# Kernel optimization log

Measured on AMD Instinct MI355X. Metric: run time of the kernel, lower is better.

## Reference

```python
import jax, jax.numpy as jnp
import numpy as np
import math

DIM = 1024
HEADS = 16
WINDOW = 256  # window_size; also used as block size (band covers 3 blocks)


def _rope(x):
    # canonical half-split RoPE over the FULL feature dim (as the module applies
    # it before the head split), base 10000
    b, s, d = x.shape
    half = d // 2
    inv_freq = 1.0 / (10000.0 ** (jnp.arange(half, dtype=jnp.float32) / half))
    ang = jnp.arange(s, dtype=jnp.float32)[:, None] * inv_freq[None, :]  # [s, half]
    cos, sin = jnp.cos(ang), jnp.sin(ang)
    x1, x2 = x[..., :half], x[..., half:]
    return jnp.concatenate([x1 * cos - x2 * sin, x1 * sin + x2 * cos], axis=-1)


def setup_inputs() -> dict:
    key = jax.random.key(0)
    ks = jax.random.split(key, 8)
    d = DIM
    q = jax.random.normal(ks[0], (2, 4096, d), dtype=jnp.float32)
    k = jax.random.normal(ks[1], (2, 4096, d), dtype=jnp.float32)
    v = jax.random.normal(ks[2], (2, 4096, d), dtype=jnp.float32)
    wq = jax.random.normal(ks[3], (d, d), dtype=jnp.float32) * 0.02
    wk = jax.random.normal(ks[4], (d, d), dtype=jnp.float32) * 0.02
    wv = jax.random.normal(ks[5], (d, d), dtype=jnp.float32) * 0.02
    wo_w = jax.random.normal(ks[6], (d, d), dtype=jnp.float32) * 0.02
    wo_b = jnp.zeros((d,), dtype=jnp.float32)
    return {"q": q, "k": k, "v": v, "wq": wq, "wk": wk, "wv": wv,
            "wo_w": wo_w, "wo_b": wo_b}


def reference(q, k, v, wq, wk, wv, wo_w, wo_b):
    b, s, d = q.shape
    h, W = HEADS, WINDOW
    dk = d // h
    B = W                      # block size == window -> band of 3 blocks
    nb = s // B

    # projections (torch Linear: x @ W^T), then RoPE over the full dim
    qp = _rope(jnp.einsum('bsd,ed->bse', q, wq))
    kp = _rope(jnp.einsum('bsd,ed->bse', k, wk))
    vp = jnp.einsum('bsd,ed->bse', v, wv)

    # split heads -> [b, h, s, dk]
    qh = qp.reshape(b, s, h, dk).transpose(0, 2, 1, 3)
    kh = kp.reshape(b, s, h, dk).transpose(0, 2, 1, 3)
    vh = vp.reshape(b, s, h, dk).transpose(0, 2, 1, 3)

    # pad keys/values by one block on each side, gather 3-block bands
    kpad = jnp.pad(kh, ((0, 0), (0, 0), (B, B), (0, 0)))
    vpad = jnp.pad(vh, ((0, 0), (0, 0), (B, B), (0, 0)))
    kblk = kpad.reshape(b, h, nb + 2, B, dk)
    vblk = vpad.reshape(b, h, nb + 2, B, dk)
    kband = jnp.concatenate([kblk[:, :, i:i + nb] for i in range(3)], axis=3)  # [b,h,nb,3B,dk]
    vband = jnp.concatenate([vblk[:, :, i:i + nb] for i in range(3)], axis=3)

    qb = qh.reshape(b, h, nb, B, dk)
    # NOTE: original multiplies by sqrt(dim_k) (not divides) -- kept faithfully
    scores = jnp.einsum('bhnqd,bhnkd->bhnqk', qb, kband) * math.sqrt(dk)

    # band mask: key global pos = (n-1)*B + ki, query global pos = n*B + qi
    n_idx = jnp.arange(nb)[:, None, None]
    qi = jnp.arange(B)[None, :, None]
    ki = jnp.arange(3 * B)[None, None, :]
    kpos = (n_idx - 1) * B + ki
    rel = ki - B - qi  # key_pos - query_pos
    valid = (rel >= -W) & (rel <= W) & (kpos >= 0) & (kpos < s)  # [nb,B,3B]

    neg = jnp.asarray(jnp.finfo(scores.dtype).min, scores.dtype)
    scores = jnp.where(valid[None, None], scores, neg)
    attn = jax.nn.softmax(scores, axis=-1)

    out = jnp.einsum('bhnqk,bhnkd->bhnqd', attn, vband)
    out = out.reshape(b, h, s, dk).transpose(0, 2, 1, 3).reshape(b, s, d)
    return jnp.einsum('bsd,ed->bse', out, wo_w) + wo_b
```

## Files before the change

### kernel.cpp

```cpp
#include <hip/hip_runtime.h>


typedef __attribute__((ext_vector_type(8))) short short8v;
typedef __attribute__((ext_vector_type(4))) float float4v;

#define MFMA16(A_, B_, C_) __builtin_amdgcn_mfma_f32_16x16x32_bf16((A_), (B_), (C_), 0, 0, 0)

__device__ __forceinline__ unsigned short f2bf_rne(float f) {
    unsigned int u = __float_as_uint(f);
    u += 0x7fffu + ((u >> 16) & 1u);
    return (unsigned short)(u >> 16);
}
__device__ __forceinline__ float bfbits2f(unsigned short h) {
    return __uint_as_float(((unsigned int)h) << 16);
}
__device__ __forceinline__ void split2(float x, short& h, short& l) {
    unsigned short hb = f2bf_rne(x);
    h = (short)hb;
    l = (short)f2bf_rne(x - bfbits2f(hb));
}

__global__ __launch_bounds__(256) void wsplit_k(
    const float* __restrict__ wq, const float* __restrict__ wk,
    unsigned short* __restrict__ o)
{
    int idx = blockIdx.x * 256 + threadIdx.x;
    const int MSK = (1 << 20) - 1;
    const float* src = (idx <= MSK) ? wq : wk;
    unsigned int base = (idx <= MSK) ? 0u : (2u << 20);
    int i = idx & MSK;
    short hh, ll;
    split2(src[i], hh, ll);
    o[base + i] = (unsigned short)hh;
    o[base + (1 << 20) + i] = (unsigned short)ll;
}

__global__ __launch_bounds__(256) void gemm_qk(
    const float* __restrict__ A0, const short* __restrict__ Bh0,
    const short* __restrict__ Bl0, float* __restrict__ C0,
    const float* __restrict__ A1, const short* __restrict__ Bh1,
    const short* __restrict__ Bl1, float* __restrict__ C1)
{
    const int N = 1024, K = 1024;
    const float* Ap = blockIdx.z ? A1 : A0;
    const short* Bhp = blockIdx.z ? Bh1 : Bh0;
    const short* Blp = blockIdx.z ? Bl1 : Bl0;
    float*       Cp = blockIdx.z ? C1 : C0;

    __shared__ __align__(16) short Ahs[128 * 32];
    __shared__ __align__(16) short Als[128 * 32];
    __shared__ __align__(16) short Bhs[128 * 32];
    __shared__ __align__(16) short Bls[128 * 32];

    const int t = threadIdx.x;
    const int bm = blockIdx.y << 7;
    const int bn = blockIdx.x << 7;
    const int lane = t & 63;
    const int wave = t >> 6;
    const int wm = (wave >> 1) << 6;
    const int wn = (wave & 1) << 6;
    const int c16 = lane & 15;
    const int quad = lane >> 4;
    const int lr = t >> 2;
    const int lc = (t & 3) << 3;

    float4v acc[4][4];
#pragma unroll
    for (int i = 0; i < 4; i++)
#pragma unroll
        for (int j = 0; j < 4; j++) acc[i][j] = (float4v){0.f, 0.f, 0.f, 0.f};

    for (int kb = 0; kb < K; kb += 32) {
#pragma unroll
        for (int g = 0; g < 2; g++) {
            const float* src = Ap + (size_t)(bm + g * 64 + lr) * K + kb + lc;
            float4v f0 = *(const float4v*)src;
            float4v f1 = *(const float4v*)(src + 4);
            short8v h, l;
#pragma unroll
            for (int j = 0; j < 8; j++) {
                float x = (j < 4) ? f0[j] : f1[j - 4];
                short hh, ll; split2(x, hh, ll);
                h[j] = hh; l[j] = ll;
            }
            *(short8v*)(Ahs + (g * 64 + lr) * 32 + lc) = h;
            *(short8v*)(Als + (g * 64 + lr) * 32 + lc) = l;
        }
#pragma unroll
        for (int g = 0; g < 2; g++) {
            size_t off = (size_t)(bn + g * 64 + lr) * K + kb + lc;
            *(short8v*)(Bhs + (g * 64 + lr) * 32 + lc) = *(const short8v*)(Bhp + off);
            *(short8v*)(Bls + (g * 64 + lr) * 32 + lc) = *(const short8v*)(Blp + off);
        }
        __syncthreads();

        short8v ah[4], al[4], bh[4], bl[4];
#pragma unroll
        for (int i = 0; i < 4; i++) {
            ah[i] = *(const short8v*)(Ahs + (wm + i * 16 + c16) * 32 + quad * 8);
            al[i] = *(const short8v*)(Als + (wm + i * 16 + c16) * 32 + quad * 8);
        }
#pragma unroll
        for (int j = 0; j < 4; j++) {
            bh[j] = *(const short8v*)(Bhs + (wn + j * 16 + c16) * 32 + quad * 8);
            bl[j] = *(const short8v*)(Bls + (wn + j * 16 + c16) * 32 + quad * 8);
        }
#pragma unroll
        for (int i = 0; i < 4; i++)
#pragma unroll
            for (int j = 0; j < 4; j++) {
                acc[i][j] = MFMA16(ah[i], bh[j], acc[i][j]);
                acc[i][j] = MFMA16(ah[i], bl[j], acc[i][j]);
                acc[i][j] = MFMA16(al[i], bh[j], acc[i][j]);
            }
        __syncthreads();
    }

#pragma unroll
    for (int i = 0; i < 4; i++)
#pragma unroll
        for (int j = 0; j < 4; j++)
#pragma unroll
            for (int r = 0; r < 4; r++) {
                int gr = bm + wm + i * 16 + quad * 4 + r;
                int gc = bn + wn + j * 16 + c16;
                Cp[(size_t)gr * N + gc] = acc[i][j][r];
            }
}

template <int MODE>
__global__ __launch_bounds__(256) void gemm_k(
    const void* __restrict__ Ap, const float* __restrict__ Bp, void* __restrict__ Cp,
    const float* __restrict__ bias)
{
    const int N = 1024, K = 1024;

    __shared__ __align__(16) short Ahs[128 * 32];
    __shared__ __align__(16) short Bhs[128 * 32];

    const int t = threadIdx.x;
    const int bm = blockIdx.y << 7;
    const int bn = blockIdx.x << 7;
    const int lane = t & 63;
    const int wave = t >> 6;
    const int wm = (wave >> 1) << 6;
    const int wn = (wave & 1) << 6;
    const int c16 = lane & 15;
    const int quad = lane >> 4;
    const int lr = t >> 2;
    const int lc = (t & 3) << 3;

    float4v acc[4][4];
#pragma unroll
    for (int i = 0; i < 4; i++)
#pragma unroll
        for (int j = 0; j < 4; j++) acc[i][j] = (float4v){0.f, 0.f, 0.f, 0.f};

    for (int kb = 0; kb < K; kb += 32) {
        if (MODE == 2) {
            const short* Ab = (const short*)Ap;
#pragma unroll
            for (int g = 0; g < 2; g++)
                *(short8v*)(Ahs + (g * 64 + lr) * 32 + lc) =
                    *(const short8v*)(Ab + (size_t)(bm + g * 64 + lr) * K + kb + lc);
        } else {
            const float* Af = (const float*)Ap;
#pragma unroll
            for (int g = 0; g < 2; g++) {
                const float* src = Af + (size_t)(bm + g * 64 + lr) * K + kb + lc;
                float4v f0 = *(const float4v*)src;
                float4v f1 = *(const float4v*)(src + 4);
                short8v h;
#pragma unroll
                for (int j = 0; j < 8; j++) h[j] = (short)f2bf_rne((j < 4) ? f0[j] : f1[j - 4]);
                *(short8v*)(Ahs + (g * 64 + lr) * 32 + lc) = h;
            }
        }
#pragma unroll
        for (int g = 0; g < 2; g++) {
            const float* src = Bp + (size_t)(bn + g * 64 + lr) * K + kb + lc;
            float4v f0 = *(const float4v*)src;
            float4v f1 = *(const float4v*)(src + 4);
            short8v h;
#pragma unroll
            for (int j = 0; j < 8; j++) h[j] = (short)f2bf_rne((j < 4) ? f0[j] : f1[j - 4]);
            *(short8v*)(Bhs + (g * 64 + lr) * 32 + lc) = h;
        }
        __syncthreads();

        short8v ah[4], bh[4];
#pragma unroll
        for (int i = 0; i < 4; i++)
            ah[i] = *(const short8v*)(Ahs + (wm + i * 16 + c16) * 32 + quad * 8);
#pragma unroll
        for (int j = 0; j < 4; j++)
            bh[j] = *(const short8v*)(Bhs + (wn + j * 16 + c16) * 32 + quad * 8);
#pragma unroll
        for (int i = 0; i < 4; i++)
#pragma unroll
            for (int j = 0; j < 4; j++)
                acc[i][j] = MFMA16(ah[i], bh[j], acc[i][j]);
        __syncthreads();
    }

#pragma unroll
    for (int i = 0; i < 4; i++)
#pragma unroll
        for (int j = 0; j < 4; j++)
#pragma unroll
            for (int r = 0; r < 4; r++) {
                int gr = bm + wm + i * 16 + quad * 4 + r;
                int gc = bn + wn + j * 16 + c16;
                float vv = acc[i][j][r];
                if (MODE == 1) {
                    ((unsigned short*)Cp)[((size_t)(gc << 1) + (gr >> 12)) * 4096 + (gr & 4095)] = f2bf_rne(vv);
                } else {
                    ((float*)Cp)[(size_t)gr * N + gc] = vv + bias[gc];
                }
            }
}

__global__ __launch_bounds__(256) void rope_pack(float* __restrict__ QP, float* __restrict__ KP)
{
    int rix = blockIdx.x & 8191;
    float* row = ((blockIdx.x >> 13) ? KP : QP) + ((size_t)rix << 10);
    int sp = rix & 4095;
    int t = threadIdx.x;

    float y1[2], y2[2];
#pragma unroll
    for (int p = 0; p < 2; p++) {
        int j = t + p * 256;
        float x1 = row[j], x2 = row[j + 512];
        float freq = __expf(-0.017988946f * (float)j);
        float ang = (float)sp * freq;
        float c, sn;
        sincosf(ang, &sn, &c);
        y1[p] = x1 * c - x2 * sn;
        y2[p] = x1 * sn + x2 * c;
    }
    __syncthreads();
    unsigned short* u = (unsigned short*)row;
#pragma unroll
    for (int p = 0; p < 2; p++) {
        int j = t + p * 256;
        short h1, l1, h2, l2;
        split2(y1[p], h1, l1);
        split2(y2[p], h2, l2);
        u[j] = (unsigned short)h1;
        u[j + 512] = (unsigned short)h2;
        u[1024 + j] = (unsigned short)l1;
        u[1024 + j + 512] = (unsigned short)l2;
    }
}

__global__ __launch_bounds__(256) void attn_k(
    const unsigned short* __restrict__ QHL, const unsigned short* __restrict__ KHL,
    const unsigned short* __restrict__ VT, unsigned short* __restrict__ AO)
{
    const int S = 4096;
    const float NEG = -1e30f;
    const int bq = blockIdx.x, h = blockIdx.y, b = blockIdx.z;
    const int t = threadIdx.x;
    const int wave = t >> 6, lane = t & 63;
    const int col = lane & 15, quad = lane >> 4;
    const int qg = (bq << 6) + (wave << 4);

    __shared__ __align__(16) short Khs[64 * 72];
    __shared__ __align__(16) short Kls[64 * 72];
    __shared__ __align__(16) short Vs[64 * 72];
    __shared__ __align__(16) short Ps[4][16 * 72];
    short* myP = &Ps[wave][0];

    const int sk = t >> 3;
    const int sd = (t & 7) << 3;

    short8v qh[2], ql[2];
    {
        const unsigned short* qr = QHL + ((size_t)(b * S + qg + col) << 11) + h * 64 + quad * 8;
        qh[0] = *(const short8v*)(qr);
        qh[1] = *(const short8v*)(qr + 32);
        ql[0] = *(const short8v*)(qr + 1024);
        ql[1] = *(const short8v*)(qr + 1024 + 32);
    }

    float mrun[4], lrun[4];
    float4v O[4];
#pragma unroll
    for (int r = 0; r < 4; r++) { mrun[r] = NEG; lrun[r] = 0.f; }
#pragma unroll
    for (int t4 = 0; t4 < 4; t4++) O[t4] = (float4v){0.f, 0.f, 0.f, 0.f};

    const int blk0 = bq << 6;
    const int kstart = (blk0 - 256 > 0) ? (blk0 - 256) : 0;
    const int kend = (blk0 + 320 < S) ? (blk0 + 320) : S;

    for (int kb = kstart; kb < kend; kb += 64) {
#pragma unroll
        for (int p = 0; p < 2; p++) {
            int key = p * 32 + sk;
            const unsigned short* krow = KHL + ((size_t)(b * S + kb + key) << 11) + h * 64 + sd;
            *(short8v*)(Khs + key * 72 + sd) = *(const short8v*)krow;
            *(short8v*)(Kls + key * 72 + sd) = *(const short8v*)(krow + 1024);
            int dm = p * 32 + sk;
            const unsigned short* vrow = VT + ((size_t)((h * 64 + dm) << 1) + b) * S + kb + sd;
            *(short8v*)(Vs + dm * 72 + sd) = *(const short8v*)vrow;
        }
        __syncthreads();

        float4v sv[4];
#pragma unroll
        for (int c = 0; c < 4; c++) {
            const short* kro = Khs + (c * 16 + col) * 72 + quad * 8;
            const short* klo = Kls + (c * 16 + col) * 72 + quad * 8;
            short8v kh0 = *(const short8v*)kro;
            short8v kh1 = *(const short8v*)(kro + 32);
            short8v kl0 = *(const short8v*)klo;
            short8v kl1 = *(const short8v*)(klo + 32);
            float4v sc = (float4v){0.f, 0.f, 0.f, 0.f};
            sc = MFMA16(qh[0], kh0, sc);
            sc = MFMA16(qh[1], kh1, sc);
            sc = MFMA16(qh[0], kl0, sc);
            sc = MFMA16(qh[1], kl1, sc);
            sc = MFMA16(ql[0], kh0, sc);
            sc = MFMA16(ql[1], kh1, sc);
            sv[c] = sc;
        }

        float mx[4], alpha[4], psum[4];
#pragma unroll
        for (int r = 0; r < 4; r++) {
            int qrow = qg + quad * 4 + r;
            float m = NEG;
#pragma unroll
            for (int c = 0; c < 4; c++) {
                int key = kb + c * 16 + col;
                float vv = (key >= qrow - 256 && key <= qrow + 256) ? sv[c][r] * 8.0f : NEG;
                sv[c][r] = vv;
                m = fmaxf(m, vv);
            }
            mx[r] = m;
        }
#pragma unroll
        for (int st = 1; st < 16; st <<= 1)
#pragma unroll
            for (int r = 0; r < 4; r++) mx[r] = fmaxf(mx[r], __shfl_xor(mx[r], st, 64));

#pragma unroll
        for (int r = 0; r < 4; r++) {
            float mn = fmaxf(mrun[r], mx[r]);
            alpha[r] = __expf(mrun[r] - mn);
            mrun[r] = mn;
            float ps = 0.f;
#pragma unroll
            for (int c = 0; c < 4; c++) {
                float p = __expf(sv[c][r] - mn);
                ps += p;
                myP[(quad * 4 + r) * 72 + c * 16 + col] = (short)f2bf_rne(p);
            }
            psum[r] = ps;
        }
#pragma unroll
        for (int st = 1; st < 16; st <<= 1)
#pragma unroll
            for (int r = 0; r < 4; r++) psum[r] += __shfl_xor(psum[r], st, 64);
#pragma unroll
        for (int r = 0; r < 4; r++) lrun[r] = lrun[r] * alpha[r] + psum[r];
#pragma unroll
        for (int t4 = 0; t4 < 4; t4++)
#pragma unroll
            for (int r = 0; r < 4; r++) O[t4][r] *= alpha[r];

#pragma unroll
        for (int kf = 0; kf < 2; kf++) {
            short8v pa = *(const short8v*)(myP + col * 72 + kf * 32 + quad * 8);
#pragma unroll
            for (int t4 = 0; t4 < 4; t4++) {
                short8v vb = *(const short8v*)(Vs + (t4 * 16 + col) * 72 + kf * 32 + quad * 8);
                O[t4] = MFMA16(pa, vb, O[t4]);
            }
        }
        __syncthreads();
    }

#pragma unroll
    for (int r = 0; r < 4; r++) {
        float inv = (lrun[r] > 0.f) ? (1.0f / lrun[r]) : 0.f;
        unsigned short* orow = AO + (size_t)(b * S + qg + quad * 4 + r) * 1024 + h * 64;
#pragma unroll
        for (int t4 = 0; t4 < 4; t4++) orow[t4 * 16 + col] = f2bf_rne(O[t4][r] * inv);
    }
}

extern "C" void kernel_launch(void* const* d_in, const int* in_sizes, int n_in,
                              void* d_out, int out_size, void* d_ws, size_t ws_size,
                              hipStream_t stream) {
    const float* q   = (const float*)d_in[0];
    const float* k   = (const float*)d_in[1];
    const float* v   = (const float*)d_in[2];
    const float* wq  = (const float*)d_in[3];
    const float* wk  = (const float*)d_in[4];
    const float* wv  = (const float*)d_in[5];
    const float* wo  = (const float*)d_in[6];
    const float* wob = (const float*)d_in[7];

    float* QP = (float*)d_ws;
    float* KP = QP + (size_t)8192 * 1024;
    unsigned short* VT = (unsigned short*)(KP + (size_t)8192 * 1024);
    unsigned short* AO = VT + (size_t)8192 * 1024;
    unsigned short* WS = VT;

    const short* wqh = (const short*)(WS);
    const short* wql = (const short*)(WS + (1u << 20));
    const short* wkh = (const short*)(WS + (2u << 20));
    const short* wkl = (const short*)(WS + (3u << 20));

    wsplit_k<<<8192, 256, 0, stream>>>(wq, wk, WS);
    gemm_qk<<<dim3(8, 64, 2), 256, 0, stream>>>(q, wqh, wql, QP, k, wkh, wkl, KP);
    rope_pack<<<16384, 256, 0, stream>>>(QP, KP);
    gemm_k<1><<<dim3(8, 64, 1), 256, 0, stream>>>(v, wv, (void*)VT, nullptr);
    attn_k<<<dim3(64, 16, 2), 256, 0, stream>>>((const unsigned short*)QP,
                                                (const unsigned short*)KP, VT, AO);
    gemm_k<2><<<dim3(8, 64, 1), 256, 0, stream>>>(AO, wo, d_out, wob);
}
```

Baseline: 468.3 us.

## Switch V/out GEMMs to fp16 with async LDS loads and batch RoPE rows

Several changes land together. The V weight is pre-converted to fp16 in a merged prep kernel, with scratch space moved into the output buffer. B-operand and pre-converted A-operand tiles are loaded straight into LDS via global_load_lds. The V-projection, P·V and output-projection paths switch from bf16 to fp16 MFMA, with P scaled by 512 to keep its range. RoPE now handles four rows per block so each sincos is reused, and the hi/lo split uses truncation for the low part. These cut conversion work and register staging, at the cost of some precision and a layout assumption in the LDS DMA writes.

```diff
diff --git a/kernel.cpp b/kernel.cpp
--- a/kernel.cpp
+++ b/kernel.cpp
@@ -3,36 +3,45 @@
 
 typedef __attribute__((ext_vector_type(8))) short short8v;
 typedef __attribute__((ext_vector_type(4))) float float4v;
-
-#define MFMA16(A_, B_, C_) __builtin_amdgcn_mfma_f32_16x16x32_bf16((A_), (B_), (C_), 0, 0, 0)
-
-__device__ __forceinline__ unsigned short f2bf_rne(float f) {
-    unsigned int u = __float_as_uint(f);
+typedef __attribute__((ext_vector_type(8))) _Float16 half8v;
+
+#define MFMA_BF16(A_, B_, C_) __builtin_amdgcn_mfma_f32_16x16x32_bf16((A_), (B_), (C_), 0, 0, 0)
+#define MFMA_F16(A_, B_, C_)  __builtin_amdgcn_mfma_f32_16x16x32_f16((A_), (B_), (C_), 0, 0, 0)
+
+__device__ __forceinline__ void split_rn(float x, short& h, short& l) {
+    unsigned int u = __float_as_uint(x);
     u += 0x7fffu + ((u >> 16) & 1u);
-    return (unsigned short)(u >> 16);
-}
-__device__ __forceinline__ float bfbits2f(unsigned short h) {
-    return __uint_as_float(((unsigned int)h) << 16);
-}
-__device__ __forceinline__ void split2(float x, short& h, short& l) {
-    unsigned short hb = f2bf_rne(x);
-    h = (short)hb;
-    l = (short)f2bf_rne(x - bfbits2f(hb));
-}
-
-__global__ __launch_bounds__(256) void wsplit_k(
+    unsigned int hb = u & 0xffff0000u;
+    h = (short)(hb >> 16);
+    float lo = x - __uint_as_float(hb);
+    l = (short)(__float_as_uint(lo) >> 16);
+}
+
+__device__ __forceinline__ void dma16(const void* g, void* l) {
+    __builtin_amdgcn_global_load_lds(
+        (__attribute__((address_space(1))) void*)g,
+        (__attribute__((address_space(3))) void*)l, 16, 0, 0);
+}
+
+__global__ __launch_bounds__(256) void prep_k(
     const float* __restrict__ wq, const float* __restrict__ wk,
-    unsigned short* __restrict__ o)
+    const float* __restrict__ wv, unsigned short* __restrict__ scr)
 {
-    int idx = blockIdx.x * 256 + threadIdx.x;
-    const int MSK = (1 << 20) - 1;
-    const float* src = (idx <= MSK) ? wq : wk;
-    unsigned int base = (idx <= MSK) ? 0u : (2u << 20);
-    int i = idx & MSK;
-    short hh, ll;
-    split2(src[i], hh, ll);
-    o[base + i] = (unsigned short)hh;
-    o[base + (1 << 20) + i] = (unsigned short)ll;
+    const int M1 = 1 << 20;
+    unsigned int tid = blockIdx.x * 256 + threadIdx.x;
+    if (tid < (unsigned)M1) {
+        short h, l; split_rn(wq[tid], h, l);
+        scr[tid] = (unsigned short)h;
+        scr[M1 + tid] = (unsigned short)l;
+    } else if (tid < (unsigned)(2 * M1)) {
+        unsigned int i = tid - M1;
+        short h, l; split_rn(wk[i], h, l);
+        scr[2 * M1 + i] = (unsigned short)h;
+        scr[3 * M1 + i] = (unsigned short)l;
+    } else {
+        unsigned int i = tid - 2 * M1;
+        scr[4 * M1 + i] = __builtin_bit_cast(unsigned short, (_Float16)wv[i]);
+    }
 }
 
 __global__ __launch_bounds__(256) void gemm_qk(
@@ -73,6 +82,12 @@
     for (int kb = 0; kb < K; kb += 32) {
 #pragma unroll
         for (int g = 0; g < 2; g++) {
+            size_t off = (size_t)(bn + g * 64 + lr) * K + kb + lc;
+            dma16(Bhp + off, Bhs + g * 2048 + wave * 512);
+            dma16(Blp + off, Bls + g * 2048 + wave * 512);
+        }
+#pragma unroll
+        for (int g = 0; g < 2; g++) {
             const float* src = Ap + (size_t)(bm + g * 64 + lr) * K + kb + lc;
             float4v f0 = *(const float4v*)src;
             float4v f1 = *(const float4v*)(src + 4);
@@ -80,17 +95,11 @@
 #pragma unroll
             for (int j = 0; j < 8; j++) {
                 float x = (j < 4) ? f0[j] : f1[j - 4];
-                short hh, ll; split2(x, hh, ll);
+                short hh, ll; split_rn(x, hh, ll);
                 h[j] = hh; l[j] = ll;
             }
             *(short8v*)(Ahs + (g * 64 + lr) * 32 + lc) = h;
             *(short8v*)(Als + (g * 64 + lr) * 32 + lc) = l;
-        }
-#pragma unroll
-        for (int g = 0; g < 2; g++) {
-            size_t off = (size_t)(bn + g * 64 + lr) * K + kb + lc;
-            *(short8v*)(Bhs + (g * 64 + lr) * 32 + lc) = *(const short8v*)(Bhp + off);
-            *(short8v*)(Bls + (g * 64 + lr) * 32 + lc) = *(const short8v*)(Blp + off);
         }
         __syncthreads();
 
@@ -109,9 +118,9 @@
         for (int i = 0; i < 4; i++)
 #pragma unroll
             for (int j = 0; j < 4; j++) {
-                acc[i][j] = MFMA16(ah[i], bh[j], acc[i][j]);
-                acc[i][j] = MFMA16(ah[i], bl[j], acc[i][j]);
-                acc[i][j] = MFMA16(al[i], bh[j], acc[i][j]);
+                acc[i][j] = MFMA_BF16(ah[i], bh[j], acc[i][j]);
+                acc[i][j] = MFMA_BF16(ah[i], bl[j], acc[i][j]);
+                acc[i][j] = MFMA_BF16(al[i], bh[j], acc[i][j]);
             }
         __syncthreads();
     }
@@ -128,15 +137,15 @@
             }
 }
 
-template <int MODE>
-__global__ __launch_bounds__(256) void gemm_k(
-    const void* __restrict__ Ap, const float* __restrict__ Bp, void* __restrict__ Cp,
-    const float* __restrict__ bias)
+template <int AF16, int BF16, int OMODE>
+__global__ __launch_bounds__(256) void gemm16(
+    const void* __restrict__ Ap, const void* __restrict__ Bp,
+    void* __restrict__ Cp, const float* __restrict__ bias)
 {
     const int N = 1024, K = 1024;
 
-    __shared__ __align__(16) short Ahs[128 * 32];
-    __shared__ __align__(16) short Bhs[128 * 32];
+    __shared__ __align__(16) short As[128 * 32];
+    __shared__ __align__(16) short Bs[128 * 32];
 
     const int t = threadIdx.x;
     const int bm = blockIdx.y << 7;
@@ -157,12 +166,12 @@
         for (int j = 0; j < 4; j++) acc[i][j] = (float4v){0.f, 0.f, 0.f, 0.f};
 
     for (int kb = 0; kb < K; kb += 32) {
-        if (MODE == 2) {
-            const short* Ab = (const short*)Ap;
+        if (AF16) {
+            const _Float16* Af = (const _Float16*)Ap;
 #pragma unroll
             for (int g = 0; g < 2; g++)
-                *(short8v*)(Ahs + (g * 64 + lr) * 32 + lc) =
-                    *(const short8v*)(Ab + (size_t)(bm + g * 64 + lr) * K + kb + lc);
+                dma16(Af + (size_t)(bm + g * 64 + lr) * K + kb + lc,
+                      As + g * 2048 + wave * 512);
         } else {
             const float* Af = (const float*)Ap;
 #pragma unroll
@@ -170,36 +179,45 @@
                 const float* src = Af + (size_t)(bm + g * 64 + lr) * K + kb + lc;
                 float4v f0 = *(const float4v*)src;
                 float4v f1 = *(const float4v*)(src + 4);
-                short8v h;
-#pragma unroll
-                for (int j = 0; j < 8; j++) h[j] = (short)f2bf_rne((j < 4) ? f0[j] : f1[j - 4]);
-                *(short8v*)(Ahs + (g * 64 + lr) * 32 + lc) = h;
-            }
-        }
-#pragma unroll
-        for (int g = 0; g < 2; g++) {
-            const float* src = Bp + (size_t)(bn + g * 64 + lr) * K + kb + lc;
-            float4v f0 = *(const float4v*)src;
-            float4v f1 = *(const float4v*)(src + 4);
-            short8v h;
-#pragma unroll
-            for (int j = 0; j < 8; j++) h[j] = (short)f2bf_rne((j < 4) ? f0[j] : f1[j - 4]);
-            *(short8v*)(Bhs + (g * 64 + lr) * 32 + lc) = h;
-        }
-        __syncthreads();
-
-        short8v ah[4], bh[4];
+                half8v h;
+#pragma unroll
+                for (int j = 0; j < 8; j++) h[j] = (_Float16)((j < 4) ? f0[j] : f1[j - 4]);
+                *(half8v*)(As + (g * 64 + lr) * 32 + lc) = h;
+            }
+        }
+        if (BF16) {
+            const _Float16* Bf = (const _Float16*)Bp;
+#pragma unroll
+            for (int g = 0; g < 2; g++)
+                dma16(Bf + (size_t)(bn + g * 64 + lr) * K + kb + lc,
+                      Bs + g * 2048 + wave * 512);
+        } else {
+            const float* Bf = (const float*)Bp;
+#pragma unroll
+            for (int g = 0; g < 2; g++) {
+                const float* src = Bf + (size_t)(bn + g * 64 + lr) * K + kb + lc;
+                float4v f0 = *(const float4v*)src;
+                float4v f1 = *(const float4v*)(src + 4);
+                half8v h;
+#pragma unroll
+                for (int j = 0; j < 8; j++) h[j] = (_Float16)((j < 4) ? f0[j] : f1[j - 4]);
+                *(half8v*)(Bs + (g * 64 + lr) * 32 + lc) = h;
+            }
+        }
+        __syncthreads();
+
+        half8v ah[4], bh[4];
 #pragma unroll
         for (int i = 0; i < 4; i++)
-            ah[i] = *(const short8v*)(Ahs + (wm + i * 16 + c16) * 32 + quad * 8);
+            ah[i] = *(const half8v*)(As + (wm + i * 16 + c16) * 32 + quad * 8);
 #pragma unroll
         for (int j = 0; j < 4; j++)
-            bh[j] = *(const short8v*)(Bhs + (wn + j * 16 + c16) * 32 + quad * 8);
+            bh[j] = *(const half8v*)(Bs + (wn + j * 16 + c16) * 32 + quad * 8);
 #pragma unroll
         for (int i = 0; i < 4; i++)
 #pragma unroll
             for (int j = 0; j < 4; j++)
-                acc[i][j] = MFMA16(ah[i], bh[j], acc[i][j]);
+                acc[i][j] = MFMA_F16(ah[i], bh[j], acc[i][j]);
         __syncthreads();
     }
 
@@ -212,8 +230,9 @@
                 int gr = bm + wm + i * 16 + quad * 4 + r;
                 int gc = bn + wn + j * 16 + c16;
                 float vv = acc[i][j][r];
-                if (MODE == 1) {
-                    ((unsigned short*)Cp)[((size_t)(gc << 1) + (gr >> 12)) * 4096 + (gr & 4095)] = f2bf_rne(vv);
+                if (OMODE == 0) {
+                    ((unsigned short*)Cp)[((size_t)(gc << 1) + (gr >> 12)) * 4096 + (gr & 4095)] =
+                        __builtin_bit_cast(unsigned short, (_Float16)vv);
                 } else {
                     ((float*)Cp)[(size_t)gr * N + gc] = vv + bias[gc];
                 }
@@ -222,35 +241,42 @@
 
 __global__ __launch_bounds__(256) void rope_pack(float* __restrict__ QP, float* __restrict__ KP)
 {
-    int rix = blockIdx.x & 8191;
-    float* row = ((blockIdx.x >> 13) ? KP : QP) + ((size_t)rix << 10);
-    int sp = rix & 4095;
+    int sp = blockIdx.x;
     int t = threadIdx.x;
-
-    float y1[2], y2[2];
+    float* rows[4] = { QP + ((size_t)sp << 10), QP + ((size_t)(4096 + sp) << 10),
+                       KP + ((size_t)sp << 10), KP + ((size_t)(4096 + sp) << 10) };
+
+    float c[2], sn[2];
+    float x1[4][2], x2[4][2];
 #pragma unroll
     for (int p = 0; p < 2; p++) {
         int j = t + p * 256;
-        float x1 = row[j], x2 = row[j + 512];
         float freq = __expf(-0.017988946f * (float)j);
         float ang = (float)sp * freq;
-        float c, sn;
-        sincosf(ang, &sn, &c);
-        y1[p] = x1 * c - x2 * sn;
-        y2[p] = x1 * sn + x2 * c;
+        sincosf(ang, &sn[p], &c[p]);
+#pragma unroll
+        for (int r = 0; r < 4; r++) {
+            x1[r][p] = rows[r][j];
+            x2[r][p] = rows[r][j + 512];
+        }
     }
     __syncthreads();
-    unsigned short* u = (unsigned short*)row;
-#pragma unroll
-    for (int p = 0; p < 2; p++) {
-        int j = t + p * 256;
-        short h1, l1, h2, l2;
-        split2(y1[p], h1, l1);
-        split2(y2[p], h2, l2);
-        u[j] = (unsigned short)h1;
-        u[j + 512] = (unsigned short)h2;
-        u[1024 + j] = (unsigned short)l1;
-        u[1024 + j + 512] = (unsigned short)l2;
+#pragma unroll
+    for (int r = 0; r < 4; r++) {
+        unsigned short* u = (unsigned short*)rows[r];
+#pragma unroll
+        for (int p = 0; p < 2; p++) {
+            int j = t + p * 256;
+            float y1 = x1[r][p] * c[p] - x2[r][p] * sn[p];
+            float y2 = x1[r][p] * sn[p] + x2[r][p] * c[p];
+            short h1, l1, h2, l2;
+            split_rn(y1, h1, l1);
+            split_rn(y2, h2, l2);
+            u[j] = (unsigned short)h1;
+            u[j + 512] = (unsigned short)h2;
+            u[1024 + j] = (unsigned short)l1;
+            u[1024 + j + 512] = (unsigned short)l2;
+        }
     }
 }
 
@@ -260,6 +286,7 @@
 {
     const int S = 4096;
     const float NEG = -1e30f;
+    const float PSC = 512.0f;
     const int bq = blockIdx.x, h = blockIdx.y, b = blockIdx.z;
     const int t = threadIdx.x;
     const int wave = t >> 6, lane = t & 63;
@@ -318,12 +345,12 @@
             short8v kl0 = *(const short8v*)klo;
             short8v kl1 = *(const short8v*)(klo + 32);
             float4v sc = (float4v){0.f, 0.f, 0.f, 0.f};
-            sc = MFMA16(qh[0], kh0, sc);
-            sc = MFMA16(qh[1], kh1, sc);
-            sc = MFMA16(qh[0], kl0, sc);
-            sc = MFMA16(qh[1], kl1, sc);
-            sc = MFMA16(ql[0], kh0, sc);
-            sc = MFMA16(ql[1], kh1, sc);
+            sc = MFMA_BF16(qh[0], kh0, sc);
+            sc = MFMA_BF16(qh[1], kh1, sc);
+            sc = MFMA_BF16(qh[0], kl0, sc);
+            sc = MFMA_BF16(qh[1], kl1, sc);
+            sc = MFMA_BF16(ql[0], kh0, sc);
+            sc = MFMA_BF16(ql[1], kh1, sc);
             sv[c] = sc;
         }
 
@@ -356,7 +383,8 @@
             for (int c = 0; c < 4; c++) {
                 float p = __expf(sv[c][r] - mn);
                 ps += p;
-                myP[(quad * 4 + r) * 72 + c * 16 + col] = (short)f2bf_rne(p);
+                myP[(quad * 4 + r) * 72 + c * 16 + col] =
+                    __builtin_bit_cast(short, (_Float16)(p * PSC));
             }
             psum[r] = ps;
         }
@@ -373,11 +401,11 @@
 
 #pragma unroll
         for (int kf = 0; kf < 2; kf++) {
-            short8v pa = *(const short8v*)(myP + col * 72 + kf * 32 + quad * 8);
+            half8v pa = *(const half8v*)(myP + col * 72 + kf * 32 + quad * 8);
 #pragma unroll
             for (int t4 = 0; t4 < 4; t4++) {
-                short8v vb = *(const short8v*)(Vs + (t4 * 16 + col) * 72 + kf * 32 + quad * 8);
-                O[t4] = MFMA16(pa, vb, O[t4]);
+                half8v vb = *(const half8v*)(Vs + (t4 * 16 + col) * 72 + kf * 32 + quad * 8);
+                O[t4] = MFMA_F16(pa, vb, O[t4]);
             }
         }
         __syncthreads();
@@ -385,10 +413,11 @@
 
 #pragma unroll
     for (int r = 0; r < 4; r++) {
-        float inv = (lrun[r] > 0.f) ? (1.0f / lrun[r]) : 0.f;
+        float inv = (lrun[r] > 0.f) ? (1.0f / (lrun[r] * PSC)) : 0.f;
         unsigned short* orow = AO + (size_t)(b * S + qg + quad * 4 + r) * 1024 + h * 64;
 #pragma unroll
-        for (int t4 = 0; t4 < 4; t4++) orow[t4 * 16 + col] = f2bf_rne(O[t4][r] * inv);
+        for (int t4 = 0; t4 < 4; t4++)
+            orow[t4 * 16 + col] = __builtin_bit_cast(unsigned short, (_Float16)(O[t4][r] * inv));
     }
 }
 
@@ -408,18 +437,20 @@
     float* KP = QP + (size_t)8192 * 1024;
     unsigned short* VT = (unsigned short*)(KP + (size_t)8192 * 1024);
     unsigned short* AO = VT + (size_t)8192 * 1024;
-    unsigned short* WS = VT;
-
-    const short* wqh = (const short*)(WS);
-    const short* wql = (const short*)(WS + (1u << 20));
-    const short* wkh = (const short*)(WS + (2u << 20));
-    const short* wkl = (const short*)(WS + (3u << 20));
-
-    wsplit_k<<<8192, 256, 0, stream>>>(wq, wk, WS);
+
+    unsigned short* scr = (unsigned short*)d_out;
+    const int M1 = 1 << 20;
+    const short* wqh = (const short*)(scr);
+    const short* wql = (const short*)(scr + M1);
+    const short* wkh = (const short*)(scr + 2 * M1);
+    const short* wkl = (const short*)(scr + 3 * M1);
+    const void*  wv16 = (const void*)(scr + 4 * M1);
+
+    prep_k<<<12288, 256, 0, stream>>>(wq, wk, wv, scr);
     gemm_qk<<<dim3(8, 64, 2), 256, 0, stream>>>(q, wqh, wql, QP, k, wkh, wkl, KP);
-    rope_pack<<<16384, 256, 0, stream>>>(QP, KP);
-    gemm_k<1><<<dim3(8, 64, 1), 256, 0, stream>>>(v, wv, (void*)VT, nullptr);
+    rope_pack<<<4096, 256, 0, stream>>>(QP, KP);
+    gemm16<0, 1, 0><<<dim3(8, 64), 256, 0, stream>>>(v, wv16, (void*)VT, nullptr);
     attn_k<<<dim3(64, 16, 2), 256, 0, stream>>>((const unsigned short*)QP,
                                                 (const unsigned short*)KP, VT, AO);
-    gemm_k<2><<<dim3(8, 64, 1), 256, 0, stream>>>(AO, wo, d_out, wob);
-}
+    gemm16<1, 0, 1><<<dim3(8, 64), 256, 0, stream>>>(AO, wo, d_out, wob);
+}
```

Measured after the change: 461.6 us. About the same (-1.4%).
